# Kernel tuning notes

Measured on AMD Instinct MI355X. Metric: run time of the kernel, lower is better.

## Reference

```python
import jax, jax.numpy as jnp
import numpy as np

B, T, E, C, I = 4, 2048, 8, 1024, 2048

def setup_inputs() -> dict:
    key = jax.random.key(0)
    k1, k2, k3, k4 = jax.random.split(key, 4)
    x = jax.random.normal(k1, (B, T, C), dtype=jnp.float32)
    routing_weights = jax.random.uniform(k2, (B, T, E), dtype=jnp.float32)
    w1 = jax.random.normal(k3, (E, C, I), dtype=jnp.float32)
    w2 = jax.random.normal(k4, (E, I, C), dtype=jnp.float32)
    return {"x": x, "routing_weights": routing_weights, "w1": w1, "w2": w2}

def reference(x, routing_weights, w1, w2):
    # [B,T,C] x [E,C,I] -> [B,T,E,I]
    h = jnp.einsum('btc,eci->btei', x, w1)
    h = jax.nn.gelu(h, approximate=False)  # torch F.gelu default is exact erf
    # [B,T,E,I] x [E,I,C] -> [B,T,E,C]
    experts_out = jnp.einsum('btei,eic->btec', h, w2)
    # weighted combine over experts -> [B,T,C]
    agg = jnp.einsum('btec,bte->btc', experts_out, routing_weights)
    return (agg, experts_out)
```

## Files before the change

kernel.cpp:

```cpp
#include <hip/hip_runtime.h>
#include <hip/hip_bf16.h>


typedef unsigned short u16;
typedef __bf16 v8bf __attribute__((ext_vector_type(8)));
typedef float  v4f  __attribute__((ext_vector_type(4)));

#define M_TOT 8192
#define E_DIM 8
#define C_DIM 1024
#define I_DIM 2048

__device__ inline u16 f2b(float f) {
    __hip_bfloat16 h = __float2bfloat16(f);
    return *reinterpret_cast<u16*>(&h);
}

__device__ inline float fast_gelu(float x) {
    float x2 = x * x;
    float z  = x * fmaf(0.0356774081f, x2, 0.7978845608f);
    float u  = __expf(2.0f * z);
    float th = fmaf(-2.0f, __builtin_amdgcn_rcpf(u + 1.0f), 1.0f);
    return 0.5f * x * (1.0f + th);
}

__device__ inline void gload16(const u16* g, u16* l) {
    __builtin_amdgcn_global_load_lds(
        (const __attribute__((address_space(1))) void*)g,
        (__attribute__((address_space(3))) void*)l,
        16, 0, 0);
}


__global__ __launch_bounds__(256) void cvt_x_kernel(const float* __restrict__ x,
                                                    u16* __restrict__ xb) {
    int idx = blockIdx.x * 256 + threadIdx.x;
    float4 v = reinterpret_cast<const float4*>(x)[idx];
    ushort4 o;
    o.x = f2b(v.x); o.y = f2b(v.y); o.z = f2b(v.z); o.w = f2b(v.w);
    reinterpret_cast<ushort4*>(xb)[idx] = o;
}

__global__ __launch_bounds__(256) void transpose_cvt_kernel(const float* __restrict__ in,
                                                            u16* __restrict__ out,
                                                            int R, int Cd) {
    __shared__ float tile[32][33];
    int e = blockIdx.z;
    const float* ip = in + (size_t)e * R * Cd;
    u16* op = out + (size_t)e * R * Cd;
    int c0 = blockIdx.x * 32, r0 = blockIdx.y * 32;
    int tx = threadIdx.x & 31;
    int ty = threadIdx.x >> 5;
#pragma unroll
    for (int k = 0; k < 4; k++)
        tile[ty + 8 * k][tx] = ip[(size_t)(r0 + ty + 8 * k) * Cd + c0 + tx];
    __syncthreads();
#pragma unroll
    for (int k = 0; k < 4; k++)
        op[(size_t)(c0 + ty + 8 * k) * R + r0 + tx] = f2b(tile[tx][ty + 8 * k]);
}

template<int K>
__device__ inline void gemm_core(const u16* __restrict__ A, const u16* __restrict__ Bt,
                                 u16* ldsA, u16* ldsB, int m0, int n0, v4f (&acc)[8][4]) {
    constexpr int NS = K / 32;
    const int t = threadIdx.x, w = t >> 6, l = t & 63;
    const int wm = w >> 2, wn = w & 3;

    const u16* asrc[2]; const u16* bsrc[2]; int adst[2];
#pragma unroll
    for (int u = 0; u < 2; ++u) {
        int f = u * 8192 + w * 1024 + l * 16;
        int g = f ^ (((f >> 7) & 3) << 4);
        int row = g >> 6, col = (g >> 1) & 31;
        asrc[u] = A  + (size_t)(m0 + row) * K + col;
        bsrc[u] = Bt + (size_t)(n0 + row) * K + col;
        adst[u] = u * 4096 + w * 512;
    }

    const int lr = l & 15, lk = l >> 4;
    int aoffE[8], boffE[4];
#pragma unroll
    for (int i = 0; i < 8; ++i) {
        int g = (wm * 128 + i * 16 + lr) * 64 + lk * 16;
        aoffE[i] = (g ^ (((g >> 7) & 3) << 4)) >> 1;
    }
#pragma unroll
    for (int j = 0; j < 4; ++j) {
        int g = (wn * 64 + j * 16 + lr) * 64 + lk * 16;
        boffE[j] = (g ^ (((g >> 7) & 3) << 4)) >> 1;
    }

    auto STAGE_A = [&](int ks) {
        u16* la = ldsA + (ks & 3) * 8192;
        int ko = ks * 32;
        gload16(asrc[0] + ko, la + adst[0]);
        gload16(asrc[1] + ko, la + adst[1]);
    };
    auto STAGE_B = [&](int ks) {
        u16* lb = ldsB + (ks & 3) * 8192;
        int ko = ks * 32;
        gload16(bsrc[0] + ko, lb + adst[0]);
        gload16(bsrc[1] + ko, lb + adst[1]);
    };

#pragma unroll
    for (int i = 0; i < 8; ++i)
#pragma unroll
        for (int j = 0; j < 4; ++j) acc[i][j] = (v4f){0.f, 0.f, 0.f, 0.f};

    STAGE_A(0); STAGE_B(0); STAGE_A(1); STAGE_B(1); STAGE_A(2); STAGE_B(2);
    asm volatile("s_waitcnt vmcnt(8)" ::: "memory");
    __builtin_amdgcn_s_barrier();

    for (int s = 0; s < NS; ++s) {
        const u16* as = ldsA + (s & 3) * 8192;
        const u16* bs = ldsB + (s & 3) * 8192;
        v8bf af[8], bfr[4];
#pragma unroll
        for (int i = 0; i < 4; ++i) af[i] = *(const v8bf*)(as + aoffE[i]);
#pragma unroll
        for (int j = 0; j < 4; ++j) bfr[j] = *(const v8bf*)(bs + boffE[j]);
        if (s < NS - 3) STAGE_A(s + 3);
        __builtin_amdgcn_s_barrier();
        asm volatile("s_waitcnt lgkmcnt(0)" ::: "memory");
        __builtin_amdgcn_s_setprio(1);
#pragma unroll
        for (int i = 0; i < 4; ++i)
#pragma unroll
            for (int j = 0; j < 4; ++j)
                acc[i][j] = __builtin_amdgcn_mfma_f32_16x16x32_bf16(af[i], bfr[j], acc[i][j], 0, 0, 0);
        __builtin_amdgcn_s_setprio(0);
        __builtin_amdgcn_s_barrier();
#pragma unroll
        for (int i = 4; i < 8; ++i) af[i] = *(const v8bf*)(as + aoffE[i]);
        if (s < NS - 3) STAGE_B(s + 3);
        __builtin_amdgcn_s_barrier();
        asm volatile("s_waitcnt lgkmcnt(0)" ::: "memory");
        __builtin_amdgcn_s_setprio(1);
#pragma unroll
        for (int i = 4; i < 8; ++i)
#pragma unroll
            for (int j = 0; j < 4; ++j)
                acc[i][j] = __builtin_amdgcn_mfma_f32_16x16x32_bf16(af[i], bfr[j], acc[i][j], 0, 0, 0);
        __builtin_amdgcn_s_setprio(0);
        if (s < NS - 3)       asm volatile("s_waitcnt vmcnt(8)" ::: "memory");
        else if (s == NS - 3) asm volatile("s_waitcnt vmcnt(4)" ::: "memory");
        else if (s == NS - 2) asm volatile("s_waitcnt vmcnt(0)" ::: "memory");
        if (s < NS - 1) __builtin_amdgcn_s_barrier();
    }
}

__global__ __launch_bounds__(512, 2) void gemm1_kernel(const u16* __restrict__ A,
                                                       const u16* __restrict__ w1T,
                                                       u16* __restrict__ H,
                                                       int e_base, int nE, size_t h_stride) {
    __shared__ __align__(16) u16 lds[65536];
    int id = blockIdx.x;
    int e, j;
    if (nE == E_DIM) { e = id & 7; j = id >> 3; }
    else             { e = e_base; j = id; }
    int n0 = (j & 7) * 256;
    int m0 = (j >> 3) * 256;
    const u16* Bt = w1T + (size_t)e * I_DIM * C_DIM;
    u16* Hp = H + (size_t)(e - e_base) * h_stride;

    v4f acc[8][4];
    gemm_core<C_DIM>(A, Bt, lds, lds + 32768, m0, n0, acc);

    int l = threadIdx.x & 63, w = threadIdx.x >> 6;
    int wm = w >> 2, wn = w & 3;
    int lr4 = (l >> 4) * 4, lc = l & 15;
#pragma unroll
    for (int i = 0; i < 8; ++i) {
        int mg = m0 + wm * 128 + i * 16 + lr4;
#pragma unroll
        for (int j2 = 0; j2 < 4; ++j2) {
            int ng = n0 + wn * 64 + j2 * 16 + lc;
#pragma unroll
            for (int r = 0; r < 4; ++r)
                Hp[(size_t)(mg + r) * I_DIM + ng] = f2b(fast_gelu(acc[i][j2][r]));
        }
    }
}

__global__ __launch_bounds__(512, 2) void gemm2_kernel(const u16* __restrict__ H,
                                                       const u16* __restrict__ w2T,
                                                       float* __restrict__ EO,
                                                       int e_base, int nE, size_t h_stride) {
    __shared__ __align__(16) u16 lds[65536];
    int id = blockIdx.x;
    int e, j;
    if (nE == E_DIM) { e = id & 7; j = id >> 3; }
    else             { e = e_base; j = id; }
    int n0 = (j & 3) * 256;
    int m0 = (j >> 2) * 256;
    const u16* A  = H + (size_t)(e - e_base) * h_stride;
    const u16* Bt = w2T + (size_t)e * C_DIM * I_DIM;

    v4f acc[8][4];
    gemm_core<I_DIM>(A, Bt, lds, lds + 32768, m0, n0, acc);

    int l = threadIdx.x & 63, w = threadIdx.x >> 6;
    int wm = w >> 2, wn = w & 3;
    int lr4 = (l >> 4) * 4, lc = l & 15;
#pragma unroll
    for (int i = 0; i < 8; ++i) {
        int mg = m0 + wm * 128 + i * 16 + lr4;
#pragma unroll
        for (int j2 = 0; j2 < 4; ++j2) {
            int ng = n0 + wn * 64 + j2 * 16 + lc;
#pragma unroll
            for (int r = 0; r < 4; ++r)
                EO[((size_t)(mg + r) * E_DIM + e) * C_DIM + ng] = acc[i][j2][r];
        }
    }
}

__global__ __launch_bounds__(256) void combine_kernel(const float* __restrict__ EO,
                                                      const float* __restrict__ Rw,
                                                      float* __restrict__ agg) {
    int idx = blockIdx.x * 256 + threadIdx.x;
    int m = idx >> 8, cq = idx & 255;
    const float4* eo4 = reinterpret_cast<const float4*>(EO);
    float4 s = make_float4(0.f, 0.f, 0.f, 0.f);
#pragma unroll
    for (int e = 0; e < E_DIM; e++) {
        float r = Rw[m * E_DIM + e];
        float4 v = eo4[((size_t)m * E_DIM + e) * 256 + cq];
        s.x += r * v.x; s.y += r * v.y; s.z += r * v.z; s.w += r * v.w;
    }
    reinterpret_cast<float4*>(agg)[(size_t)m * 256 + cq] = s;
}

extern "C" void kernel_launch(void* const* d_in, const int* in_sizes, int n_in,
                              void* d_out, int out_size, void* d_ws, size_t ws_size,
                              hipStream_t stream) {
    const float* x  = (const float*)d_in[0];
    const float* rw = (const float*)d_in[1];
    const float* w1 = (const float*)d_in[2];
    const float* w2 = (const float*)d_in[3];

    float* agg = (float*)d_out;
    float* EO  = agg + (size_t)M_TOT * C_DIM;

    u16* xb  = (u16*)d_ws;
    u16* w1T = xb  + (size_t)M_TOT * C_DIM;
    u16* w2T = w1T + (size_t)E_DIM * I_DIM * C_DIM;
    u16* h   = w2T + (size_t)E_DIM * C_DIM * I_DIM;

    size_t elems_before_h = (size_t)M_TOT * C_DIM + 2 * (size_t)E_DIM * I_DIM * C_DIM;
    size_t h_per_expert   = (size_t)M_TOT * I_DIM;
    bool batched = ws_size >= (elems_before_h + (size_t)E_DIM * h_per_expert) * sizeof(u16);

    cvt_x_kernel<<<(M_TOT * C_DIM) / 1024, 256, 0, stream>>>(x, xb);
    transpose_cvt_kernel<<<dim3(I_DIM / 32, C_DIM / 32, E_DIM), 256, 0, stream>>>(w1, w1T, C_DIM, I_DIM);
    transpose_cvt_kernel<<<dim3(C_DIM / 32, I_DIM / 32, E_DIM), 256, 0, stream>>>(w2, w2T, I_DIM, C_DIM);

    if (batched) {
        gemm1_kernel<<<E_DIM * 8 * 32, 512, 0, stream>>>(xb, w1T, h, 0, E_DIM, h_per_expert);
        gemm2_kernel<<<E_DIM * 4 * 32, 512, 0, stream>>>(h, w2T, EO, 0, E_DIM, h_per_expert);
    } else {
        for (int e = 0; e < E_DIM; e++) {
            gemm1_kernel<<<8 * 32, 512, 0, stream>>>(xb, w1T, h, e, 1, 0);
            gemm2_kernel<<<4 * 32, 512, 0, stream>>>(h, w2T, EO, e, 1, 0);
        }
    }

    combine_kernel<<<M_TOT, 256, 0, stream>>>(EO, rw, agg);
}
```

Measured before the change: 1.005 ms.

## Restructure GEMM main loop into 64-wide K tiles with 4-phase quadrant schedule

Changes the GEMM core from a 4-slot ring buffer with 32-wide K steps and 3-stage prefetch to double-buffered 64-wide K tiles. Each tile is computed in four barrier-separated phases over output quadrants, interleaving register fragment reads and global prefetch issue with MFMA bursts under raised priority. sched_barriers pin the ordering. The aim is fewer loop iterations, fewer vmcnt waits and a better LDS-read/MFMA overlap. In exchange, prefetch depth drops to one tile ahead with a full vmcnt(0) wait per tile.

```diff
diff --git a/kernel.cpp b/kernel.cpp
--- a/kernel.cpp
+++ b/kernel.cpp
@@ -60,11 +60,19 @@
         op[(size_t)(c0 + ty + 8 * k) * R + r0 + tx] = f2b(tile[tx][ty + 8 * k]);
 }
 
+#define PH_PRE  __builtin_amdgcn_s_barrier();                            \
+                asm volatile("s_waitcnt lgkmcnt(0)" ::: "memory");       \
+                __builtin_amdgcn_sched_barrier(0);                       \
+                __builtin_amdgcn_s_setprio(1);
+#define PH_POST __builtin_amdgcn_s_setprio(0);                           \
+                __builtin_amdgcn_sched_barrier(0);                       \
+                __builtin_amdgcn_s_barrier();
+
 template<int K>
 __device__ inline void gemm_core(const u16* __restrict__ A, const u16* __restrict__ Bt,
                                  u16* ldsA, u16* ldsB, int m0, int n0, v4f (&acc)[8][4]) {
-    constexpr int NS = K / 32;
-    const int t = threadIdx.x, w = t >> 6, l = t & 63;
+    constexpr int NT = K / 64;
+    const int t0 = threadIdx.x, w = t0 >> 6, l = t0 & 63;
     const int wm = w >> 2, wn = w & 3;
 
     const u16* asrc[2]; const u16* bsrc[2]; int adst[2];
@@ -109,45 +117,88 @@
 #pragma unroll
         for (int j = 0; j < 4; ++j) acc[i][j] = (v4f){0.f, 0.f, 0.f, 0.f};
 
-    STAGE_A(0); STAGE_B(0); STAGE_A(1); STAGE_B(1); STAGE_A(2); STAGE_B(2);
-    asm volatile("s_waitcnt vmcnt(8)" ::: "memory");
+    STAGE_A(0); STAGE_A(1); STAGE_B(0); STAGE_B(1);
+    asm volatile("s_waitcnt vmcnt(0)" ::: "memory");
     __builtin_amdgcn_s_barrier();
 
-    for (int s = 0; s < NS; ++s) {
-        const u16* as = ldsA + (s & 3) * 8192;
-        const u16* bs = ldsB + (s & 3) * 8192;
-        v8bf af[8], bfr[4];
-#pragma unroll
-        for (int i = 0; i < 4; ++i) af[i] = *(const v8bf*)(as + aoffE[i]);
-#pragma unroll
-        for (int j = 0; j < 4; ++j) bfr[j] = *(const v8bf*)(bs + boffE[j]);
-        if (s < NS - 3) STAGE_A(s + 3);
-        __builtin_amdgcn_s_barrier();
-        asm volatile("s_waitcnt lgkmcnt(0)" ::: "memory");
-        __builtin_amdgcn_s_setprio(1);
+    for (int t = 0; t < NT; ++t) {
+        const u16* a0 = ldsA + ((t & 1) * 2) * 8192;
+        const u16* a1 = a0 + 8192;
+        const u16* b0 = ldsB + ((t & 1) * 2) * 8192;
+        const u16* b1 = b0 + 8192;
+        const bool pf = (t < NT - 1);
+        v8bf af0[4], af1[4];
+        v8bf b00[2], b01[2];
+        v8bf b10[2], b11[2];
+
+#pragma unroll
+        for (int i = 0; i < 4; ++i) {
+            af0[i] = *(const v8bf*)(a0 + aoffE[i]);
+            af1[i] = *(const v8bf*)(a1 + aoffE[i]);
+        }
+#pragma unroll
+        for (int j = 0; j < 2; ++j) {
+            b00[j] = *(const v8bf*)(b0 + boffE[j]);
+            b01[j] = *(const v8bf*)(b1 + boffE[j]);
+        }
+        if (pf) STAGE_A(2 * t + 2);
+        PH_PRE
 #pragma unroll
         for (int i = 0; i < 4; ++i)
 #pragma unroll
-            for (int j = 0; j < 4; ++j)
-                acc[i][j] = __builtin_amdgcn_mfma_f32_16x16x32_bf16(af[i], bfr[j], acc[i][j], 0, 0, 0);
+            for (int j = 0; j < 2; ++j) {
+                acc[i][j] = __builtin_amdgcn_mfma_f32_16x16x32_bf16(af0[i], b00[j], acc[i][j], 0, 0, 0);
+                acc[i][j] = __builtin_amdgcn_mfma_f32_16x16x32_bf16(af1[i], b01[j], acc[i][j], 0, 0, 0);
+            }
+        PH_POST
+
+#pragma unroll
+        for (int j = 0; j < 2; ++j) {
+            b10[j] = *(const v8bf*)(b0 + boffE[2 + j]);
+            b11[j] = *(const v8bf*)(b1 + boffE[2 + j]);
+        }
+        if (pf) STAGE_A(2 * t + 3);
+        PH_PRE
+#pragma unroll
+        for (int i = 0; i < 4; ++i)
+#pragma unroll
+            for (int j = 0; j < 2; ++j) {
+                acc[i][2 + j] = __builtin_amdgcn_mfma_f32_16x16x32_bf16(af0[i], b10[j], acc[i][2 + j], 0, 0, 0);
+                acc[i][2 + j] = __builtin_amdgcn_mfma_f32_16x16x32_bf16(af1[i], b11[j], acc[i][2 + j], 0, 0, 0);
+            }
+        PH_POST
+
+#pragma unroll
+        for (int i = 0; i < 4; ++i) {
+            af0[i] = *(const v8bf*)(a0 + aoffE[4 + i]);
+            af1[i] = *(const v8bf*)(a1 + aoffE[4 + i]);
+        }
+        if (pf) STAGE_B(2 * t + 2);
+        PH_PRE
+#pragma unroll
+        for (int i = 0; i < 4; ++i)
+#pragma unroll
+            for (int j = 0; j < 2; ++j) {
+                acc[4 + i][2 + j] = __builtin_amdgcn_mfma_f32_16x16x32_bf16(af0[i], b10[j], acc[4 + i][2 + j], 0, 0, 0);
+                acc[4 + i][2 + j] = __builtin_amdgcn_mfma_f32_16x16x32_bf16(af1[i], b11[j], acc[4 + i][2 + j], 0, 0, 0);
+            }
+        PH_POST
+
+        if (pf) STAGE_B(2 * t + 3);
+        PH_PRE
+#pragma unroll
+        for (int i = 0; i < 4; ++i)
+#pragma unroll
+            for (int j = 0; j < 2; ++j) {
+                acc[4 + i][j] = __builtin_amdgcn_mfma_f32_16x16x32_bf16(af0[i], b00[j], acc[4 + i][j], 0, 0, 0);
+                acc[4 + i][j] = __builtin_amdgcn_mfma_f32_16x16x32_bf16(af1[i], b01[j], acc[4 + i][j], 0, 0, 0);
+            }
         __builtin_amdgcn_s_setprio(0);
-        __builtin_amdgcn_s_barrier();
-#pragma unroll
-        for (int i = 4; i < 8; ++i) af[i] = *(const v8bf*)(as + aoffE[i]);
-        if (s < NS - 3) STAGE_B(s + 3);
-        __builtin_amdgcn_s_barrier();
-        asm volatile("s_waitcnt lgkmcnt(0)" ::: "memory");
-        __builtin_amdgcn_s_setprio(1);
-#pragma unroll
-        for (int i = 4; i < 8; ++i)
-#pragma unroll
-            for (int j = 0; j < 4; ++j)
-                acc[i][j] = __builtin_amdgcn_mfma_f32_16x16x32_bf16(af[i], bfr[j], acc[i][j], 0, 0, 0);
-        __builtin_amdgcn_s_setprio(0);
-        if (s < NS - 3)       asm volatile("s_waitcnt vmcnt(8)" ::: "memory");
-        else if (s == NS - 3) asm volatile("s_waitcnt vmcnt(4)" ::: "memory");
-        else if (s == NS - 2) asm volatile("s_waitcnt vmcnt(0)" ::: "memory");
-        if (s < NS - 1) __builtin_amdgcn_s_barrier();
+        __builtin_amdgcn_sched_barrier(0);
+        if (pf) {
+            asm volatile("s_waitcnt vmcnt(0)" ::: "memory");
+            __builtin_amdgcn_s_barrier();
+        }
     }
 }
 
```

Result: faster. 981.7 us (-2.3%).
